# Optimization experiments

Measured on AMD Instinct MI355X. Metric: run time of the kernel, lower is better.

## Reference

```python
import jax, jax.numpy as jnp
import numpy as np

N, IN_DIM, OUT_DIM = 8192, 256, 128
NEG_BIG = -9e15


def setup_inputs() -> dict:
    key = jax.random.key(0)
    k_x, k_a, k_w, k_att = jax.random.split(key, 4)
    X = jax.random.normal(k_x, (N, IN_DIM), dtype=jnp.float32)
    A = jax.random.randint(k_a, (N, N), 0, 2).astype(jnp.float32)
    # nn.Linear(in_dim, out_dim, bias=False): weight [out_dim, in_dim]
    W = jax.random.normal(k_w, (OUT_DIM, IN_DIM), dtype=jnp.float32) / np.sqrt(IN_DIM)
    # nn.Linear(out_dim, 1, bias=False): weight [1, out_dim] -> store as [out_dim]
    a_w = jax.random.normal(k_att, (OUT_DIM,), dtype=jnp.float32) / np.sqrt(OUT_DIM)
    return {"X": X, "A": A, "W": W, "a_w": a_w}


def reference(X, A, W, a_w):
    Wh = X @ W.T                                  # [N, out_dim]
    e = jax.nn.relu(Wh) @ a_w                      # [N]  (a(relu(Wh)).squeeze(-1))
    # NOTE: faithful to source: e broadcasts over rows -> score[i, j] = e[j]
    scores = jnp.where(A > 0, e[None, :], NEG_BIG)  # [N, N]
    attention = jax.nn.softmax(scores, axis=1)      # [N, N]
    h_prime = attention @ Wh                        # [N, out_dim]
    return jax.nn.relu(h_prime)
```

## Files before the change

kernel.cpp:

```cpp
#include <hip/hip_runtime.h>

typedef float        f32x4  __attribute__((ext_vector_type(4)));
typedef __bf16       bf16x8 __attribute__((ext_vector_type(8)));
typedef __bf16       bf16x4 __attribute__((ext_vector_type(4)));
typedef unsigned int u32x4  __attribute__((ext_vector_type(4)));

#define NN   8192
#define IND  256
#define OUTD 128
#define NB   144
#define KSPLIT 8
#define KRANGE 1024
#define KCHUNK 128
#define BSTRIDE 136

__device__ __forceinline__ bf16x8 cvt2(f32x4 a, f32x4 b) {
  bf16x8 r;
  r[0]=(__bf16)a[0]; r[1]=(__bf16)a[1]; r[2]=(__bf16)a[2]; r[3]=(__bf16)a[3];
  r[4]=(__bf16)b[0]; r[5]=(__bf16)b[1]; r[6]=(__bf16)b[2]; r[7]=(__bf16)b[3];
  return r;
}

__global__ __launch_bounds__(256) void k1_wh_e(const float* __restrict__ X,
                                               const float* __restrict__ W,
                                               const float* __restrict__ aw,
                                               float* __restrict__ Wh,
                                               float* __restrict__ ev) {
  __shared__ float red[4][16][128];
  const int tid  = threadIdx.x;
  const int lane = tid & 63;
  const int wave = tid >> 6;
  const int nlo  = lane & 15;
  const int quad = lane >> 4;
  const int rowBase = blockIdx.x * 16;

  const float* xp = X + (size_t)(rowBase + nlo) * IND + wave * 64 + quad * 8;
  f32x4 acc[8];
#pragma unroll
  for (int nt = 0; nt < 8; ++nt) acc[nt] = f32x4{0.f, 0.f, 0.f, 0.f};

#pragma unroll
  for (int kb = 0; kb < 64; kb += 32) {
    f32x4 a0 = *(const f32x4*)(xp + kb);
    f32x4 a1 = *(const f32x4*)(xp + kb + 4);
    bf16x8 af = cvt2(a0, a1);
#pragma unroll
    for (int nt = 0; nt < 8; ++nt) {
      const float* wp = W + (size_t)(nt * 16 + nlo) * IND + wave * 64 + kb + quad * 8;
      f32x4 b0 = *(const f32x4*)wp;
      f32x4 b1 = *(const f32x4*)(wp + 4);
      acc[nt] = __builtin_amdgcn_mfma_f32_16x16x32_bf16(af, cvt2(b0, b1), acc[nt], 0, 0, 0);
    }
  }
#pragma unroll
  for (int nt = 0; nt < 8; ++nt)
#pragma unroll
    for (int rg = 0; rg < 4; ++rg)
      red[wave][quad * 4 + rg][nt * 16 + nlo] = acc[nt][rg];
  __syncthreads();

  const int r  = tid >> 4;
  const int c0 = (tid & 15) * 8;
  f32x4 vlo = *(const f32x4*)&red[0][r][c0];
  f32x4 vhi = *(const f32x4*)&red[0][r][c0 + 4];
#pragma unroll
  for (int w = 1; w < 4; ++w) {
    vlo += *(const f32x4*)&red[w][r][c0];
    vhi += *(const f32x4*)&red[w][r][c0 + 4];
  }
  *(f32x4*)(Wh + (size_t)(rowBase + r) * OUTD + c0)     = vlo;
  *(f32x4*)(Wh + (size_t)(rowBase + r) * OUTD + c0 + 4) = vhi;

  float pa = 0.f;
#pragma unroll
  for (int j = 0; j < 4; ++j) {
    pa += fmaxf(vlo[j], 0.f) * aw[c0 + j];
    pa += fmaxf(vhi[j], 0.f) * aw[c0 + 4 + j];
  }
#pragma unroll
  for (int off = 8; off; off >>= 1) pa += __shfl_xor(pa, off, 64);
  if ((tid & 15) == 0) ev[rowBase + r] = pa;
}

__global__ __launch_bounds__(256) void k2_bt(const float* __restrict__ Wh,
                                             const float* __restrict__ ev,
                                             __bf16* __restrict__ Bt) {
  const int j = blockIdx.x * 256 + threadIdx.x;
  const float w = expf(ev[j]);
  const int n0 = blockIdx.y * 18;
#pragma unroll
  for (int i = 0; i < 18; ++i) {
    const int n = n0 + i;
    float v = 0.f;
    if (n < OUTD) v = w * Wh[(size_t)j * OUTD + n];
    else if (n == OUTD) v = w;
    Bt[(size_t)n * NN + j] = (__bf16)v;
  }
}

__global__ __launch_bounds__(256, 2) void k3_partial(const float* __restrict__ Adj,
                                                     const __bf16* __restrict__ Bt,
                                                     float* __restrict__ part) {
  __shared__ unsigned short bt[NB * BSTRIDE];
  const int tid  = threadIdx.x;
  const int lane = tid & 63;
  const int wave = tid >> 6;
  const int nlo  = lane & 15;
  const int quad = lane >> 4;
  const int rowW = blockIdx.x * 64 + wave * 16;
  const int k0   = blockIdx.y * KRANGE;

  const int brow = tid >> 4;
  const int bcol = (tid & 15) * 8;

  f32x4 acc[9];
#pragma unroll
  for (int nt = 0; nt < 9; ++nt) acc[nt] = f32x4{0.f, 0.f, 0.f, 0.f};

  const float*  ap = Adj + (size_t)(rowW + nlo) * NN + quad * 8 + k0;
  const __bf16* bq = Bt + (size_t)brow * NN + k0 + bcol;

  u32x4 bregA[9];
  f32x4 aregA[8];
#pragma unroll
  for (int rr = 0; rr < 9; ++rr)
    bregA[rr] = *(const u32x4*)(bq + (size_t)(rr * 16) * NN);
#pragma unroll
  for (int s = 0; s < 4; ++s) {
    aregA[2 * s]     = __builtin_nontemporal_load((const f32x4*)(ap + s * 32));
    aregA[2 * s + 1] = __builtin_nontemporal_load((const f32x4*)(ap + s * 32 + 4));
  }

  for (int c = 0; c < KRANGE / KCHUNK; ++c) {
#pragma unroll
    for (int rr = 0; rr < 9; ++rr)
      *(u32x4*)(bt + (rr * 16 + brow) * BSTRIDE + bcol) = bregA[rr];
    __syncthreads();

    u32x4 bregB[9];
    f32x4 aregB[8];
    if (c < KRANGE / KCHUNK - 1) {
      const int kc1 = (c + 1) * KCHUNK;
#pragma unroll
      for (int rr = 0; rr < 9; ++rr)
        bregB[rr] = *(const u32x4*)(bq + (size_t)(rr * 16) * NN + kc1);
#pragma unroll
      for (int s = 0; s < 4; ++s) {
        aregB[2 * s]     = __builtin_nontemporal_load((const f32x4*)(ap + kc1 + s * 32));
        aregB[2 * s + 1] = __builtin_nontemporal_load((const f32x4*)(ap + kc1 + s * 32 + 4));
      }
    }

#pragma unroll
    for (int s = 0; s < 4; ++s) {
      bf16x8 af = cvt2(aregA[2 * s], aregA[2 * s + 1]);
      const unsigned short* bp = bt + s * 32 + quad * 8;
#pragma unroll
      for (int nt = 0; nt < 9; ++nt) {
        bf16x8 bf = *(const bf16x8*)(bp + (nt * 16 + nlo) * BSTRIDE);
        acc[nt] = __builtin_amdgcn_mfma_f32_16x16x32_bf16(af, bf, acc[nt], 0, 0, 0);
      }
    }
    __syncthreads();

    if (c < KRANGE / KCHUNK - 1) {
#pragma unroll
      for (int rr = 0; rr < 9; ++rr) bregA[rr] = bregB[rr];
#pragma unroll
      for (int s = 0; s < 8; ++s) aregA[s] = aregB[s];
    }
  }

  float* pbase = part + ((size_t)blockIdx.y * NN + rowW) * NB;
#pragma unroll
  for (int nt = 0; nt < 8; ++nt)
#pragma unroll
    for (int rg = 0; rg < 4; ++rg)
      pbase[(size_t)(quad * 4 + rg) * NB + nt * 16 + nlo] = acc[nt][rg];
  if (nlo == 0) {
#pragma unroll
    for (int rg = 0; rg < 4; ++rg)
      pbase[(size_t)(quad * 4 + rg) * NB + 128] = acc[8][rg];
  }
}

__global__ __launch_bounds__(256) void k3_reduce(const float* __restrict__ part,
                                                 float* __restrict__ out) {
  const int col = threadIdx.x & 127;
  const int row = blockIdx.x * 2 + (threadIdx.x >> 7);
  float num = 0.f, den = 0.f;
#pragma unroll
  for (int s = 0; s < KSPLIT; ++s) {
    const size_t base = ((size_t)s * NN + row) * NB;
    num += part[base + col];
    den += part[base + 128];
  }
  out[(size_t)row * OUTD + col] = fmaxf(num / den, 0.f);
}

extern "C" void kernel_launch(void* const* d_in, const int* in_sizes, int n_in,
                              void* d_out, int out_size, void* d_ws, size_t ws_size,
                              hipStream_t stream) {
  const float* X  = (const float*)d_in[0];
  const float* A  = (const float*)d_in[1];
  const float* W  = (const float*)d_in[2];
  const float* aw = (const float*)d_in[3];
  float* out = (float*)d_out;

  char* ws = (char*)d_ws;
  float*  Wh   = (float*)ws;
  float*  ev   = (float*)(ws + 4194304);
  __bf16* Bt   = (__bf16*)(ws + 4227072);
  float*  part = (float*)(ws + 8388608);

  k1_wh_e<<<512, 256, 0, stream>>>(X, W, aw, Wh, ev);
  k2_bt<<<dim3(32, 8), 256, 0, stream>>>(Wh, ev, Bt);
  k3_partial<<<dim3(128, KSPLIT), 256, 0, stream>>>(A, Bt, part);
  k3_reduce<<<4096, 256, 0, stream>>>(part, out);
}
```

Measured before the change: 415.1 us.

## Fuse Bt construction into projection kernel and stage whole K-slice of Bt in LDS

The projection kernel now computes exp(e), scales Wh and writes the transposed bf16 Bt directly, removing the separate Bt kernel and the Wh/e round-trip. The main partial kernel now uses 512 threads covering 128 rows, a 16-way K split of 512, and loads the entire 144x512 Bt slice into 144 KB of XOR-swizzled dynamic LDS once. Its inner loop then only streams the adjacency with register double-buffering and has no per-chunk barriers. In exchange, occupancy drops to one large block per CU and the partial-sum buffer doubles in size for the reduce kernel.

Result: slower. 423.9 us (+2.1%).

```diff
diff --git a/kernel.cpp b/kernel.cpp
--- a/kernel.cpp
+++ b/kernel.cpp
@@ -2,17 +2,15 @@
 
 typedef float        f32x4  __attribute__((ext_vector_type(4)));
 typedef __bf16       bf16x8 __attribute__((ext_vector_type(8)));
-typedef __bf16       bf16x4 __attribute__((ext_vector_type(4)));
 typedef unsigned int u32x4  __attribute__((ext_vector_type(4)));
 
 #define NN   8192
 #define IND  256
 #define OUTD 128
 #define NB   144
-#define KSPLIT 8
-#define KRANGE 1024
-#define KCHUNK 128
-#define BSTRIDE 136
+#define KSPLIT 16
+#define KRANGE 512
+#define BT_BYTES (144 * 1024)
 
 __device__ __forceinline__ bf16x8 cvt2(f32x4 a, f32x4 b) {
   bf16x8 r;
@@ -21,11 +19,10 @@
   return r;
 }
 
-__global__ __launch_bounds__(256) void k1_wh_e(const float* __restrict__ X,
-                                               const float* __restrict__ W,
-                                               const float* __restrict__ aw,
-                                               float* __restrict__ Wh,
-                                               float* __restrict__ ev) {
+__global__ __launch_bounds__(256) void k1_bt(const float* __restrict__ X,
+                                             const float* __restrict__ W,
+                                             const float* __restrict__ aw,
+                                             __bf16* __restrict__ Bt) {
   __shared__ float red[4][16][128];
   const int tid  = threadIdx.x;
   const int lane = tid & 63;
@@ -68,106 +65,91 @@
     vlo += *(const f32x4*)&red[w][r][c0];
     vhi += *(const f32x4*)&red[w][r][c0 + 4];
   }
-  *(f32x4*)(Wh + (size_t)(rowBase + r) * OUTD + c0)     = vlo;
-  *(f32x4*)(Wh + (size_t)(rowBase + r) * OUTD + c0 + 4) = vhi;
-
   float pa = 0.f;
 #pragma unroll
-  for (int j = 0; j < 4; ++j) {
-    pa += fmaxf(vlo[j], 0.f) * aw[c0 + j];
-    pa += fmaxf(vhi[j], 0.f) * aw[c0 + 4 + j];
+  for (int i = 0; i < 4; ++i) {
+    pa += fmaxf(vlo[i], 0.f) * aw[c0 + i];
+    pa += fmaxf(vhi[i], 0.f) * aw[c0 + 4 + i];
   }
 #pragma unroll
   for (int off = 8; off; off >>= 1) pa += __shfl_xor(pa, off, 64);
-  if ((tid & 15) == 0) ev[rowBase + r] = pa;
-}
-
-__global__ __launch_bounds__(256) void k2_bt(const float* __restrict__ Wh,
-                                             const float* __restrict__ ev,
-                                             __bf16* __restrict__ Bt) {
-  const int j = blockIdx.x * 256 + threadIdx.x;
-  const float w = expf(ev[j]);
-  const int n0 = blockIdx.y * 18;
-#pragma unroll
-  for (int i = 0; i < 18; ++i) {
-    const int n = n0 + i;
-    float v = 0.f;
-    if (n < OUTD) v = w * Wh[(size_t)j * OUTD + n];
-    else if (n == OUTD) v = w;
-    Bt[(size_t)n * NN + j] = (__bf16)v;
-  }
-}
-
-__global__ __launch_bounds__(256, 2) void k3_partial(const float* __restrict__ Adj,
-                                                     const __bf16* __restrict__ Bt,
-                                                     float* __restrict__ part) {
-  __shared__ unsigned short bt[NB * BSTRIDE];
+  const float wexp = expf(pa);
+  const int j = rowBase + r;
+
+#pragma unroll
+  for (int i = 0; i < 4; ++i)
+    Bt[(size_t)(c0 + i) * NN + j] = (__bf16)(vlo[i] * wexp);
+#pragma unroll
+  for (int i = 0; i < 4; ++i)
+    Bt[(size_t)(c0 + 4 + i) * NN + j] = (__bf16)(vhi[i] * wexp);
+  if ((tid & 15) == 0)
+    Bt[(size_t)OUTD * NN + j] = (__bf16)wexp;
+  if (tid < 120) {
+    const int row = 129 + (tid >> 3);
+    const int cc  = rowBase + (tid & 7) * 2;
+    Bt[(size_t)row * NN + cc]     = (__bf16)0.f;
+    Bt[(size_t)row * NN + cc + 1] = (__bf16)0.f;
+  }
+}
+
+__global__ __launch_bounds__(512) void k3_partial(const float* __restrict__ Adj,
+                                                  const __bf16* __restrict__ Bt,
+                                                  float* __restrict__ part) {
+  extern __shared__ char btile[];
   const int tid  = threadIdx.x;
   const int lane = tid & 63;
-  const int wave = tid >> 6;
+  const int wv   = tid >> 6;
   const int nlo  = lane & 15;
   const int quad = lane >> 4;
-  const int rowW = blockIdx.x * 64 + wave * 16;
+  const int rowW = blockIdx.x * 128 + wv * 16;
   const int k0   = blockIdx.y * KRANGE;
 
-  const int brow = tid >> 4;
-  const int bcol = (tid & 15) * 8;
+  const float* ap = Adj + (size_t)(rowW + nlo) * NN + k0 + quad * 8;
+
+  f32x4 aA[8], aB[8];
+#pragma unroll
+  for (int s4 = 0; s4 < 4; ++s4) {
+    aA[2 * s4]     = __builtin_nontemporal_load((const f32x4*)(ap + s4 * 32));
+    aA[2 * s4 + 1] = __builtin_nontemporal_load((const f32x4*)(ap + s4 * 32 + 4));
+  }
+
+#pragma unroll
+  for (int it = 0; it < 18; ++it) {
+    const int row = it * 8 + wv;
+    const int swz = (row & 7) << 4;
+    u32x4 v = *(const u32x4*)((const char*)(Bt + (size_t)row * NN + k0) + lane * 16);
+    *(u32x4*)(btile + row * 1024 + ((lane * 16) ^ swz)) = v;
+  }
+  __syncthreads();
 
   f32x4 acc[9];
 #pragma unroll
   for (int nt = 0; nt < 9; ++nt) acc[nt] = f32x4{0.f, 0.f, 0.f, 0.f};
 
-  const float*  ap = Adj + (size_t)(rowW + nlo) * NN + quad * 8 + k0;
-  const __bf16* bq = Bt + (size_t)brow * NN + k0 + bcol;
-
-  u32x4 bregA[9];
-  f32x4 aregA[8];
-#pragma unroll
-  for (int rr = 0; rr < 9; ++rr)
-    bregA[rr] = *(const u32x4*)(bq + (size_t)(rr * 16) * NN);
-#pragma unroll
-  for (int s = 0; s < 4; ++s) {
-    aregA[2 * s]     = __builtin_nontemporal_load((const f32x4*)(ap + s * 32));
-    aregA[2 * s + 1] = __builtin_nontemporal_load((const f32x4*)(ap + s * 32 + 4));
-  }
-
-  for (int c = 0; c < KRANGE / KCHUNK; ++c) {
-#pragma unroll
-    for (int rr = 0; rr < 9; ++rr)
-      *(u32x4*)(bt + (rr * 16 + brow) * BSTRIDE + bcol) = bregA[rr];
-    __syncthreads();
-
-    u32x4 bregB[9];
-    f32x4 aregB[8];
-    if (c < KRANGE / KCHUNK - 1) {
-      const int kc1 = (c + 1) * KCHUNK;
-#pragma unroll
-      for (int rr = 0; rr < 9; ++rr)
-        bregB[rr] = *(const u32x4*)(bq + (size_t)(rr * 16) * NN + kc1);
-#pragma unroll
-      for (int s = 0; s < 4; ++s) {
-        aregB[2 * s]     = __builtin_nontemporal_load((const f32x4*)(ap + kc1 + s * 32));
-        aregB[2 * s + 1] = __builtin_nontemporal_load((const f32x4*)(ap + kc1 + s * 32 + 4));
+  const int swzr = (nlo & 7) << 4;
+  for (int c = 0; c < 4; ++c) {
+    if (c < 3) {
+      const int kc1 = (c + 1) * 128;
+#pragma unroll
+      for (int s4 = 0; s4 < 4; ++s4) {
+        aB[2 * s4]     = __builtin_nontemporal_load((const f32x4*)(ap + kc1 + s4 * 32));
+        aB[2 * s4 + 1] = __builtin_nontemporal_load((const f32x4*)(ap + kc1 + s4 * 32 + 4));
       }
     }
-
-#pragma unroll
-    for (int s = 0; s < 4; ++s) {
-      bf16x8 af = cvt2(aregA[2 * s], aregA[2 * s + 1]);
-      const unsigned short* bp = bt + s * 32 + quad * 8;
+#pragma unroll
+    for (int s4 = 0; s4 < 4; ++s4) {
+      const int s = c * 4 + s4;
+      bf16x8 af = cvt2(aA[2 * s4], aA[2 * s4 + 1]);
+      const int cbl = s * 64 + quad * 16;
 #pragma unroll
       for (int nt = 0; nt < 9; ++nt) {
-        bf16x8 bf = *(const bf16x8*)(bp + (nt * 16 + nlo) * BSTRIDE);
+        bf16x8 bf = *(const bf16x8*)(btile + (nt * 16 + nlo) * 1024 + (cbl ^ swzr));
         acc[nt] = __builtin_amdgcn_mfma_f32_16x16x32_bf16(af, bf, acc[nt], 0, 0, 0);
       }
     }
-    __syncthreads();
-
-    if (c < KRANGE / KCHUNK - 1) {
-#pragma unroll
-      for (int rr = 0; rr < 9; ++rr) bregA[rr] = bregB[rr];
-#pragma unroll
-      for (int s = 0; s < 8; ++s) aregA[s] = aregB[s];
+    if (c < 3) {
+#pragma unroll
+      for (int s = 0; s < 8; ++s) aA[s] = aB[s];
     }
   }
 
@@ -208,13 +190,17 @@
   float* out = (float*)d_out;
 
   char* ws = (char*)d_ws;
-  float*  Wh   = (float*)ws;
-  float*  ev   = (float*)(ws + 4194304);
-  __bf16* Bt   = (__bf16*)(ws + 4227072);
-  float*  part = (float*)(ws + 8388608);
-
-  k1_wh_e<<<512, 256, 0, stream>>>(X, W, aw, Wh, ev);
-  k2_bt<<<dim3(32, 8), 256, 0, stream>>>(Wh, ev, Bt);
-  k3_partial<<<dim3(128, KSPLIT), 256, 0, stream>>>(A, Bt, part);
+  __bf16* Bt   = (__bf16*)ws;
+  float*  part = (float*)(ws + 4194304);
+
+  static bool attr_done = false;
+  if (!attr_done) {
+    hipFuncSetAttribute((const void*)k3_partial,
+                        hipFuncAttributeMaxDynamicSharedMemorySize, BT_BYTES);
+    attr_done = true;
+  }
+
+  k1_bt<<<512, 256, 0, stream>>>(X, W, aw, Bt);
+  k3_partial<<<dim3(64, KSPLIT), 512, BT_BYTES, stream>>>(A, Bt, part);
   k3_reduce<<<4096, 256, 0, stream>>>(part, out);
 }
```
